# Kernel tuning notes

Measured on AMD Instinct MI355X. Metric: run time of the kernel, lower is better.

The kernel has to match this reference:

```python
import jax, jax.numpy as jnp
import numpy as np

H = 12
D_MODEL = 768
D_K = D_MODEL // H  # 64


def setup_inputs() -> dict:
    key = jax.random.key(0)
    ks = jax.random.split(key, 16)
    B, S, D = 4, 1024, D_MODEL
    scale = 1.0 / np.sqrt(D)
    inp = {
        "query": jax.random.normal(ks[0], (B, S, D), jnp.float32),
        "key": jax.random.normal(ks[1], (B, S, D), jnp.float32),
        "value": jax.random.normal(ks[2], (B, S, D), jnp.float32),
        "times": jax.random.normal(ks[3], (2, B, S, D), jnp.float32),
        # learned params (Linear weights stored torch-style [out, in])
        "Wq": jax.random.normal(ks[4], (D, D), jnp.float32) * scale,
        "bq": jnp.zeros((D,), jnp.float32),
        "Wk": jax.random.normal(ks[5], (D, D), jnp.float32) * scale,
        "bk": jnp.zeros((D,), jnp.float32),
        "Wv": jax.random.normal(ks[6], (D, D), jnp.float32) * scale,
        "bv": jnp.zeros((D,), jnp.float32),
        "Wt": jax.random.normal(ks[7], (D, D), jnp.float32) * scale,
        "bt": jnp.zeros((D,), jnp.float32),
        "Wo": jax.random.normal(ks[8], (D, D), jnp.float32) * scale,
        "bo": jnp.zeros((D,), jnp.float32),
    }
    return inp


def _split_heads(x, B, S):
    # [B,S,D] -> [B,H,S,D_K]
    return x.reshape(B, S, H, D_K).transpose(0, 2, 1, 3)


def reference(query, key, value, times, Wq, bq, Wk, bk, Wv, bv, Wt, bt, Wo, bo):
    B, S, D = query.shape
    inv_sqrt_dk = 1.0 / jnp.sqrt(jnp.asarray(D_K, query.dtype))
    # q/k/v projections are identical across time-loop iterations; hoist them.
    q = _split_heads(query @ Wq.T + bq, B, S)   # [B,H,S,dk]
    k = _split_heads(key @ Wk.T + bk, B, S)
    v = _split_heads(value @ Wv.T + bv, B, S)
    x = jnp.zeros_like(q)
    n_times = times.shape[0]
    for i in range(n_times):  # small fixed loop over time embeddings
        t = _split_heads(times[i] @ Wt.T + bt, B, S)
        # dual-score attention: query.time + query.key, each scaled by 1/sqrt(d_k)
        scores = (jnp.einsum('bhqd,bhkd->bhqk', q, t)
                  + jnp.einsum('bhqd,bhkd->bhqk', q, k)) * inv_sqrt_dk
        p = jax.nn.softmax(scores, axis=-1)
        x = x + jnp.einsum('bhqk,bhkd->bhqd', p, v)
    x = x.transpose(0, 2, 1, 3).reshape(B, S, H * D_K)
    return x @ Wo.T + bo
```

## Files before the change

kernel.cpp:

```cpp
#include <hip/hip_runtime.h>
#include <hip/hip_fp16.h>

typedef _Float16 v8h __attribute__((ext_vector_type(8)));
typedef _Float16 v4h __attribute__((ext_vector_type(4)));
typedef _Float16 v2h __attribute__((ext_vector_type(2)));
typedef float v4f __attribute__((ext_vector_type(4)));

#define MFMA_F16 __builtin_amdgcn_mfma_f32_16x16x32_f16
#define EXP2F __builtin_amdgcn_exp2f

__device__ static inline v2h pkrtz(float a, float b) {
  return __builtin_bit_cast(v2h, __builtin_amdgcn_cvt_pkrtz(a, b));
}

__device__ static inline void async_copy16(const void* g, void* l) {
  __builtin_amdgcn_global_load_lds(
      (const __attribute__((address_space(1))) void*)g,
      (__attribute__((address_space(3))) void*)l, 16, 0, 0);
}

struct CastArgs {
  const float* src[10];
  _Float16* dst[10];
  int start[11];
  float scale[10];
};
__global__ void cast_all(CastArgs a) {
  const int g = blockIdx.x * 256 + threadIdx.x;
  if (g >= a.start[10]) return;
  int z = 0;
  #pragma unroll
  for (int i = 1; i < 10; ++i) if (g >= a.start[i]) z = i;
  const int i0 = g - a.start[z];
  const float sc = a.scale[z];
  const float* s = a.src[z] + (size_t)i0 * 8;
  const float4 f0 = *(const float4*)s;
  const float4 f1 = *(const float4*)(s + 4);
  v8h o = {(_Float16)(f0.x * sc), (_Float16)(f0.y * sc),
           (_Float16)(f0.z * sc), (_Float16)(f0.w * sc),
           (_Float16)(f1.x * sc), (_Float16)(f1.y * sc),
           (_Float16)(f1.z * sc), (_Float16)(f1.w * sc)};
  *(v8h*)(a.dst[z] + (size_t)i0 * 8) = o;
}

struct GemmArgs {
  const _Float16* A1[4]; const _Float16* A2[4];
  const _Float16* W1[4]; const _Float16* W2[4];
  const float* b1[4];    const float* b2[4];
  void* out[4];
  float bscale[4];
  int K[4];
  int mode[4];
};

template <int MT>
__global__ __launch_bounds__(256) void gemm_mt(GemmArgs g) {
  constexpr int iA = MT / 32;
  constexpr int NMT = MT / 32;
  __shared__ _Float16 a_lds[MT * 64];
  __shared__ _Float16 w_lds[128 * 64];
  const int z = blockIdx.z;
  const int KK = g.K[z];
  const int tid = threadIdx.x;
  const int w = tid >> 6, lane = tid & 63, quad = lane >> 4, l16 = lane & 15;
  const int m0 = blockIdx.x * MT, n0 = blockIdx.y * 128;
  const int wm = (w >> 1) * (MT / 2), wn = (w & 1) * 64;

  size_t srcOff[4]; int ldsOff[4];
  #pragma unroll
  for (int i = 0; i < 4; ++i) {
    const int c = i * 256 + tid, row = c >> 3, slot = c & 7;
    srcOff[i] = (size_t)row * 768 + (size_t)((slot ^ (row & 7)) * 8);
    ldsOff[i] = (i * 256 + w * 64) * 8;
  }

  v4f acc[NMT][4] = {};

  for (int k0 = 0; k0 < KK; k0 += 64) {
    const _Float16* Asrc = (k0 < 768) ? g.A1[z] : g.A2[z];
    const _Float16* Wsrc = (k0 < 768) ? g.W1[z] : g.W2[z];
    const int kc = (k0 < 768) ? k0 : k0 - 768;
    __syncthreads();
    #pragma unroll
    for (int i = 0; i < 4; ++i) {
      if (i < iA)
        async_copy16(Asrc + (size_t)m0 * 768 + kc + srcOff[i], &a_lds[ldsOff[i]]);
      async_copy16(Wsrc + (size_t)n0 * 768 + kc + srcOff[i], &w_lds[ldsOff[i]]);
    }
    __syncthreads();

    #pragma unroll
    for (int kh = 0; kh < 2; ++kh) {
      v8h af[NMT], bf[4];
      #pragma unroll
      for (int mt = 0; mt < NMT; ++mt) {
        const int r = wm + mt * 16 + l16;
        af[mt] = *(const v8h*)&a_lds[r * 64 + (((kh * 4 + quad) ^ (r & 7)) * 8)];
      }
      #pragma unroll
      for (int nt = 0; nt < 4; ++nt) {
        const int r = wn + nt * 16 + l16;
        bf[nt] = *(const v8h*)&w_lds[r * 64 + (((kh * 4 + quad) ^ (r & 7)) * 8)];
      }
      #pragma unroll
      for (int mt = 0; mt < NMT; ++mt)
        #pragma unroll
        for (int nt = 0; nt < 4; ++nt)
          acc[mt][nt] = MFMA_F16(af[mt], bf[nt], acc[mt][nt], 0, 0, 0);
    }
  }

  const int mode = g.mode[z];
  #pragma unroll
  for (int nt = 0; nt < 4; ++nt) {
    const int col = n0 + wn + nt * 16 + l16;
    float bv = g.b1[z][col] * g.bscale[z];
    if (g.b2[z]) bv += g.b2[z][col];
    if (mode == 1) {
      _Float16* outp = (_Float16*)g.out[z];
      const int h = col >> 6, dk = col & 63;
      #pragma unroll
      for (int mt = 0; mt < NMT; ++mt) {
        const int row = m0 + wm + mt * 16 + quad * 4;
        const int b = row >> 10, s = row & 1023;
        const int sp = (s & ~31) | ((s & 12) << 1) | ((s & 16) >> 2);
        v4h pack = {(_Float16)(acc[mt][nt][0] + bv), (_Float16)(acc[mt][nt][1] + bv),
                    (_Float16)(acc[mt][nt][2] + bv), (_Float16)(acc[mt][nt][3] + bv)};
        *(v4h*)&outp[(size_t)((b * 12 + h) * 64 + dk) * 1024 + sp] = pack;
      }
    } else {
      #pragma unroll
      for (int mt = 0; mt < NMT; ++mt)
        #pragma unroll
        for (int r = 0; r < 4; ++r) {
          const int row = m0 + wm + mt * 16 + quad * 4 + r;
          const float v = acc[mt][nt][r] + bv;
          if (mode == 2) ((float*)g.out[z])[(size_t)row * 768 + col] = v;
          else ((_Float16*)g.out[z])[(size_t)row * 768 + col] = (_Float16)v;
        }
    }
  }
}

__global__ __launch_bounds__(256) void attn(
    const _Float16* __restrict__ Q,
    const _Float16* __restrict__ KT0, const _Float16* __restrict__ KT1,
    const _Float16* __restrict__ Vt,
    _Float16* __restrict__ X)
{
  __shared__ _Float16 lds[6 * 4096];

  const int tid = threadIdx.x;
  const int w = tid >> 6, lane = tid & 63, quad = lane >> 4, l16 = lane & 15;

  const int orig = blockIdx.y * 16 + blockIdx.x;
  const int wgid = (orig & 7) * 96 + (orig >> 3);
  const int bh = wgid >> 4, q0 = (wgid & 15) * 64;
  const int b = bh / 12, h = bh % 12;
  const size_t base = (size_t)b * 1024 * 768 + h * 64;

  const _Float16* k0s = KT0 + base;
  const _Float16* k1s = KT1 + base;
  const _Float16* vs  = Vt + (size_t)bh * 64 * 1024;

  size_t ktOff[2], vOff[2]; int ldsOff[2];
  #pragma unroll
  for (int i = 0; i < 2; ++i) {
    const int c = i * 256 + w * 64 + lane, row = c >> 3, slot = c & 7;
    const int logical = slot ^ (row & 7);
    ktOff[i] = (size_t)row * 768 + (size_t)(logical * 8);
    vOff[i] = (size_t)row * 1024 + (size_t)(logical * 8);
    ldsOff[i] = c * 8;
  }
  auto stage = [&](int buf) {
    #pragma unroll
    for (int i = 0; i < 2; ++i) {
      async_copy16(k0s + ktOff[i], &lds[buf * 4096 + ldsOff[i]]);
      async_copy16(k1s + ktOff[i], &lds[8192 + buf * 4096 + ldsOff[i]]);
      async_copy16(vs + vOff[i], &lds[16384 + buf * 4096 + ldsOff[i]]);
    }
    k0s += 64 * 768; k1s += 64 * 768; vs += 64;
  };

  const _Float16* Qw = Q + base + (size_t)(q0 + w * 16) * 768;
  const v8h qf0 = *(const v8h*)(Qw + (size_t)l16 * 768 + quad * 8);
  const v8h qf1 = *(const v8h*)(Qw + (size_t)l16 * 768 + 32 + quad * 8);

  int ra0[4], ra1[4];
  #pragma unroll
  for (int t = 0; t < 4; ++t) {
    const int r = t * 16 + l16, rw = r & 7;
    ra0[t] = (r * 64 + ((quad ^ rw) * 8)) * 2;
    ra1[t] = ra0[t] ^ 64;
  }

  const _Float16 one = (_Float16)1.f;
  const v8h ones8 = {one, one, one, one, one, one, one, one};
  v4f o[2][4] = {};
  v4f osum[2] = {};

  auto body = [&](int B, bool doStage) {
    __syncthreads();
    if (doStage) stage((B == 0) ? 1 : 0);

    const char* L = (const char*)lds;

    v4f s[2][4];
    __builtin_amdgcn_s_setprio(1);
    #pragma unroll
    for (int kvt = 0; kvt < 4; ++kvt) {
      const v8h k00 = *(const v8h*)(L + B + ra0[kvt]);
      const v8h k01 = *(const v8h*)(L + B + ra1[kvt]);
      const v8h k10 = *(const v8h*)(L + 16384 + B + ra0[kvt]);
      const v8h k11 = *(const v8h*)(L + 16384 + B + ra1[kvt]);
      s[0][kvt] = MFMA_F16(k00, qf0, v4f{}, 0, 0, 0);
      s[0][kvt] = MFMA_F16(k01, qf1, s[0][kvt], 0, 0, 0);
      s[1][kvt] = MFMA_F16(k10, qf0, v4f{}, 0, 0, 0);
      s[1][kvt] = MFMA_F16(k11, qf1, s[1][kvt], 0, 0, 0);
    }
    __builtin_amdgcn_s_setprio(0);

    v8h pb8[2][2];
    #pragma unroll
    for (int t = 0; t < 2; ++t)
      #pragma unroll
      for (int gg = 0; gg < 2; ++gg) {
        const v4f sa = s[t][gg * 2], sb = s[t][gg * 2 + 1];
        const v2h a0 = pkrtz(EXP2F(sa[0]), EXP2F(sa[1]));
        const v2h a1 = pkrtz(EXP2F(sa[2]), EXP2F(sa[3]));
        const v2h b0 = pkrtz(EXP2F(sb[0]), EXP2F(sb[1]));
        const v2h b1 = pkrtz(EXP2F(sb[2]), EXP2F(sb[3]));
        pb8[t][gg] = v8h{a0[0], a0[1], a1[0], a1[1], b0[0], b0[1], b1[0], b1[1]};
        osum[t] = MFMA_F16(ones8, pb8[t][gg], osum[t], 0, 0, 0);
      }

    __builtin_amdgcn_s_setprio(1);
    #pragma unroll
    for (int dkt = 0; dkt < 4; ++dkt) {
      const v8h v0 = *(const v8h*)(L + 32768 + B + ra0[dkt]);
      const v8h v1 = *(const v8h*)(L + 32768 + B + ra1[dkt]);
      o[0][dkt] = MFMA_F16(v0, pb8[0][0], o[0][dkt], 0, 0, 0);
      o[0][dkt] = MFMA_F16(v1, pb8[0][1], o[0][dkt], 0, 0, 0);
      o[1][dkt] = MFMA_F16(v0, pb8[1][0], o[1][dkt], 0, 0, 0);
      o[1][dkt] = MFMA_F16(v1, pb8[1][1], o[1][dkt], 0, 0, 0);
    }
    __builtin_amdgcn_s_setprio(0);
  };

  stage(0);
  for (int it = 0; it < 7; ++it) {
    body(0, true);
    body(8192, true);
  }
  body(0, true);
  body(8192, false);

  const float i0 = 1.0f / osum[0][0], i1 = 1.0f / osum[1][0];

  _Float16* Xw = X + base + (size_t)(q0 + w * 16 + l16) * 768;
  #pragma unroll
  for (int dkt = 0; dkt < 4; ++dkt) {
    v4h pack;
    #pragma unroll
    for (int r = 0; r < 4; ++r)
      pack[r] = (_Float16)(o[0][dkt][r] * i0 + o[1][dkt][r] * i1);
    *(v4h*)&Xw[dkt * 16 + quad * 4] = pack;
  }
}

extern "C" void kernel_launch(void* const* d_in, const int* in_sizes, int n_in,
                              void* d_out, int out_size, void* d_ws, size_t ws_size,
                              hipStream_t stream) {
  const float* query = (const float*)d_in[0];
  const float* key   = (const float*)d_in[1];
  const float* value = (const float*)d_in[2];
  const float* times = (const float*)d_in[3];
  const float* Wq = (const float*)d_in[4];  const float* bq = (const float*)d_in[5];
  const float* Wk = (const float*)d_in[6];  const float* bk = (const float*)d_in[7];
  const float* Wv = (const float*)d_in[8];  const float* bv = (const float*)d_in[9];
  const float* Wt = (const float*)d_in[10]; const float* bt = (const float*)d_in[11];
  const float* Wo = (const float*)d_in[12]; const float* bo = (const float*)d_in[13];
  float* out = (float*)d_out;

  const size_t NELEM = (size_t)4096 * 768;
  const size_t WELEM = (size_t)768 * 768;
  const float QSCALE = 0.125f * 1.4426950408889634f;

  char* ws = (char*)d_ws;
  size_t off = 0;
  auto alloc = [&](size_t bytes) {
    void* p = ws + off; off += (bytes + 255) & ~(size_t)255; return p;
  };
  _Float16* qh  = (_Float16*)alloc(NELEM * 2);
  _Float16* kh  = (_Float16*)alloc(NELEM * 2);
  _Float16* vh  = (_Float16*)alloc(NELEM * 2);
  _Float16* wqh = (_Float16*)alloc(WELEM * 2);
  _Float16* wkh = (_Float16*)alloc(WELEM * 2);
  _Float16* wvh = (_Float16*)alloc(WELEM * 2);
  _Float16* wth = (_Float16*)alloc(WELEM * 2);
  _Float16* woh = (_Float16*)alloc(WELEM * 2);
  _Float16* Qh  = (_Float16*)alloc(NELEM * 2);
  _Float16* KT0 = (_Float16*)alloc(NELEM * 2);
  _Float16* KT1 = (_Float16*)alloc(NELEM * 2);
  _Float16* Vt  = (_Float16*)alloc(NELEM * 2);
  _Float16* t0h = (_Float16*)d_out;
  _Float16* t1h = t0h + NELEM;
  _Float16* Xh = qh;

  CastArgs ca = {};
  const int nA8 = (int)(NELEM / 8), nW8 = (int)(WELEM / 8);
  const float* csrc[10] = {query, key, value, times, times + NELEM, Wq, Wk, Wv, Wt, Wo};
  _Float16* cdst[10] = {qh, kh, vh, t0h, t1h, wqh, wkh, wvh, wth, woh};
  int acc8 = 0;
  for (int i = 0; i < 10; ++i) {
    ca.src[i] = csrc[i]; ca.dst[i] = cdst[i];
    ca.start[i] = acc8;
    acc8 += (i < 5) ? nA8 : nW8;
    ca.scale[i] = (i == 5) ? QSCALE : 1.0f;
  }
  ca.start[10] = acc8;
  cast_all<<<dim3((acc8 + 255) / 256), 256, 0, stream>>>(ca);

  GemmArgs pa = {};
  pa.A1[0] = t0h; pa.A2[0] = kh; pa.W1[0] = wth; pa.W2[0] = wkh;
  pa.b1[0] = bt; pa.b2[0] = bk; pa.out[0] = KT0; pa.bscale[0] = 1.0f;
  pa.K[0] = 1536; pa.mode[0] = 0;
  pa.A1[1] = t1h; pa.A2[1] = kh; pa.W1[1] = wth; pa.W2[1] = wkh;
  pa.b1[1] = bt; pa.b2[1] = bk; pa.out[1] = KT1; pa.bscale[1] = 1.0f;
  pa.K[1] = 1536; pa.mode[1] = 0;
  pa.A1[2] = qh; pa.A2[2] = qh; pa.W1[2] = wqh; pa.W2[2] = wqh;
  pa.b1[2] = bq; pa.b2[2] = nullptr; pa.out[2] = Qh; pa.bscale[2] = QSCALE;
  pa.K[2] = 768; pa.mode[2] = 0;
  pa.A1[3] = vh; pa.A2[3] = vh; pa.W1[3] = wvh; pa.W2[3] = wvh;
  pa.b1[3] = bv; pa.b2[3] = nullptr; pa.out[3] = Vt; pa.bscale[3] = 1.0f;
  pa.K[3] = 768; pa.mode[3] = 1;
  gemm_mt<128><<<dim3(32, 6, 4), 256, 0, stream>>>(pa);

  attn<<<dim3(16, 48), 256, 0, stream>>>(Qh, KT0, KT1, Vt, Xh);

  GemmArgs oa = {};
  oa.A1[0] = Xh; oa.A2[0] = Xh; oa.W1[0] = woh; oa.W2[0] = woh;
  oa.b1[0] = bo; oa.b2[0] = nullptr; oa.out[0] = out; oa.bscale[0] = 1.0f;
  oa.K[0] = 768; oa.mode[0] = 2;
  gemm_mt<64><<<dim3(64, 6, 1), 256, 0, stream>>>(oa);
}
```

Before: 228.6 us.

## Fuse fp32-to-fp16 activation cast into projection GEMM with double-buffered staging

Activations are no longer cast to fp16 in a separate pass. The projection GEMM now reads fp32 query/key/value/times directly, converting them in registers before writing to LDS, so the cast kernel only handles the weights. Both GEMM variants also get double-buffered LDS for W (and for A in the fp16 path), with the next tile prefetched while the current one is computed. This removes a full fp16 write and re-read of about 5 activation tensors. In exchange the GEMM issues fp32 global loads (twice the bytes per A tile), uses more registers, and adds an extra barrier per k-step.

```diff
diff --git a/kernel.cpp b/kernel.cpp
--- a/kernel.cpp
+++ b/kernel.cpp
@@ -20,17 +20,17 @@
 }
 
 struct CastArgs {
-  const float* src[10];
-  _Float16* dst[10];
-  int start[11];
-  float scale[10];
+  const float* src[5];
+  _Float16* dst[5];
+  int start[6];
+  float scale[5];
 };
 __global__ void cast_all(CastArgs a) {
   const int g = blockIdx.x * 256 + threadIdx.x;
-  if (g >= a.start[10]) return;
+  if (g >= a.start[5]) return;
   int z = 0;
   #pragma unroll
-  for (int i = 1; i < 10; ++i) if (g >= a.start[i]) z = i;
+  for (int i = 1; i < 5; ++i) if (g >= a.start[i]) z = i;
   const int i0 = g - a.start[z];
   const float sc = a.scale[z];
   const float* s = a.src[z] + (size_t)i0 * 8;
@@ -44,7 +44,7 @@
 }
 
 struct GemmArgs {
-  const _Float16* A1[4]; const _Float16* A2[4];
+  const void* A1[4]; const void* A2[4];
   const _Float16* W1[4]; const _Float16* W2[4];
   const float* b1[4];    const float* b2[4];
   void* out[4];
@@ -53,12 +53,12 @@
   int mode[4];
 };
 
-template <int MT>
+template <int MT, bool AF32>
 __global__ __launch_bounds__(256) void gemm_mt(GemmArgs g) {
-  constexpr int iA = MT / 32;
   constexpr int NMT = MT / 32;
-  __shared__ _Float16 a_lds[MT * 64];
-  __shared__ _Float16 w_lds[128 * 64];
+  constexpr int ASLOT = MT / 32;
+  __shared__ _Float16 a_lds[(AF32 ? 1 : 2) * MT * 64];
+  __shared__ _Float16 w_lds[2 * 128 * 64];
   const int z = blockIdx.z;
   const int KK = g.K[z];
   const int tid = threadIdx.x;
@@ -66,28 +66,91 @@
   const int m0 = blockIdx.x * MT, n0 = blockIdx.y * 128;
   const int wm = (w >> 1) * (MT / 2), wn = (w & 1) * 64;
 
-  size_t srcOff[4]; int ldsOff[4];
+  size_t srcOffW[4]; int ldsOffW[4];
   #pragma unroll
   for (int i = 0; i < 4; ++i) {
     const int c = i * 256 + tid, row = c >> 3, slot = c & 7;
-    srcOff[i] = (size_t)row * 768 + (size_t)((slot ^ (row & 7)) * 8);
-    ldsOff[i] = (i * 256 + w * 64) * 8;
-  }
+    srcOffW[i] = (size_t)row * 768 + (size_t)((slot ^ (row & 7)) * 8);
+    ldsOffW[i] = (i * 256 + w * 64) * 8;
+  }
+
+  auto stageW = [&](const _Float16* Wsrc, int kc, int buf) {
+    #pragma unroll
+    for (int i = 0; i < 4; ++i)
+      async_copy16(Wsrc + (size_t)n0 * 768 + kc + srcOffW[i],
+                   &w_lds[buf * 8192 + ldsOffW[i]]);
+  };
+  auto stageA16 = [&](const _Float16* Asrc, int kc, int buf) {
+    #pragma unroll
+    for (int i = 0; i < MT / 32; ++i)
+      async_copy16(Asrc + (size_t)m0 * 768 + kc + srcOffW[i],
+                   &a_lds[buf * MT * 64 + ldsOffW[i]]);
+  };
+
+  int rowA[ASLOT], colA[ASLOT], dstA[ASLOT];
+  float4 areg[ASLOT][2];
+  if constexpr (AF32) {
+    #pragma unroll
+    for (int i = 0; i < ASLOT; ++i) {
+      const int s = i * 256 + tid, row = s >> 3, slot = s & 7;
+      rowA[i] = row;
+      colA[i] = (slot ^ (row & 7)) * 8;
+      dstA[i] = s * 8;
+    }
+  }
+  auto loadA = [&](const float* Af, int kc) {
+    #pragma unroll
+    for (int i = 0; i < ASLOT; ++i) {
+      const float* p = Af + (size_t)(m0 + rowA[i]) * 768 + kc + colA[i];
+      areg[i][0] = *(const float4*)p;
+      areg[i][1] = *(const float4*)(p + 4);
+    }
+  };
+  auto writeA = [&]() {
+    #pragma unroll
+    for (int i = 0; i < ASLOT; ++i) {
+      const float4 f0 = areg[i][0], f1 = areg[i][1];
+      v8h o = {(_Float16)f0.x, (_Float16)f0.y, (_Float16)f0.z, (_Float16)f0.w,
+               (_Float16)f1.x, (_Float16)f1.y, (_Float16)f1.z, (_Float16)f1.w};
+      *(v8h*)&a_lds[dstA[i]] = o;
+    }
+  };
+
+  const void* A1 = g.A1[z]; const void* A2 = g.A2[z];
+  const _Float16* W1 = g.W1[z]; const _Float16* W2 = g.W2[z];
 
   v4f acc[NMT][4] = {};
 
+  if constexpr (AF32) loadA((const float*)A1, 0);
+  else stageA16((const _Float16*)A1, 0, 0);
+  stageW(W1, 0, 0);
+
+  int cur = 0;
   for (int k0 = 0; k0 < KK; k0 += 64) {
-    const _Float16* Asrc = (k0 < 768) ? g.A1[z] : g.A2[z];
-    const _Float16* Wsrc = (k0 < 768) ? g.W1[z] : g.W2[z];
-    const int kc = (k0 < 768) ? k0 : k0 - 768;
+    const int k0n = k0 + 64;
+    const bool has_next = k0n < KK;
+    const int kcn = (k0n < 768) ? k0n : k0n - 768;
+    const bool nfirst = k0n < 768;
+
     __syncthreads();
-    #pragma unroll
-    for (int i = 0; i < 4; ++i) {
-      if (i < iA)
-        async_copy16(Asrc + (size_t)m0 * 768 + kc + srcOff[i], &a_lds[ldsOff[i]]);
-      async_copy16(Wsrc + (size_t)n0 * 768 + kc + srcOff[i], &w_lds[ldsOff[i]]);
-    }
-    __syncthreads();
+
+    if constexpr (AF32) {
+      writeA();
+      __syncthreads();
+      if (has_next) {
+        loadA((const float*)(nfirst ? A1 : A2), kcn);
+        stageW(nfirst ? W1 : W2, kcn, cur ^ 1);
+      }
+    } else {
+      if (has_next) {
+        stageA16((const _Float16*)(nfirst ? A1 : A2), kcn, cur ^ 1);
+        stageW(nfirst ? W1 : W2, kcn, cur ^ 1);
+      }
+    }
+
+    const _Float16* al;
+    if constexpr (AF32) al = a_lds; else al = &a_lds[cur * MT * 64];
+    const _Float16* wl = &w_lds[cur * 8192];
 
     #pragma unroll
     for (int kh = 0; kh < 2; ++kh) {
@@ -95,12 +158,12 @@
       #pragma unroll
       for (int mt = 0; mt < NMT; ++mt) {
         const int r = wm + mt * 16 + l16;
-        af[mt] = *(const v8h*)&a_lds[r * 64 + (((kh * 4 + quad) ^ (r & 7)) * 8)];
+        af[mt] = *(const v8h*)&al[r * 64 + (((kh * 4 + quad) ^ (r & 7)) * 8)];
       }
       #pragma unroll
       for (int nt = 0; nt < 4; ++nt) {
         const int r = wn + nt * 16 + l16;
-        bf[nt] = *(const v8h*)&w_lds[r * 64 + (((kh * 4 + quad) ^ (r & 7)) * 8)];
+        bf[nt] = *(const v8h*)&wl[r * 64 + (((kh * 4 + quad) ^ (r & 7)) * 8)];
       }
       #pragma unroll
       for (int mt = 0; mt < NMT; ++mt)
@@ -108,6 +171,7 @@
         for (int nt = 0; nt < 4; ++nt)
           acc[mt][nt] = MFMA_F16(af[mt], bf[nt], acc[mt][nt], 0, 0, 0);
     }
+    cur ^= 1;
   }
 
   const int mode = g.mode[z];
@@ -291,9 +355,6 @@
   auto alloc = [&](size_t bytes) {
     void* p = ws + off; off += (bytes + 255) & ~(size_t)255; return p;
   };
-  _Float16* qh  = (_Float16*)alloc(NELEM * 2);
-  _Float16* kh  = (_Float16*)alloc(NELEM * 2);
-  _Float16* vh  = (_Float16*)alloc(NELEM * 2);
   _Float16* wqh = (_Float16*)alloc(WELEM * 2);
   _Float16* wkh = (_Float16*)alloc(WELEM * 2);
   _Float16* wvh = (_Float16*)alloc(WELEM * 2);
@@ -303,38 +364,36 @@
   _Float16* KT0 = (_Float16*)alloc(NELEM * 2);
   _Float16* KT1 = (_Float16*)alloc(NELEM * 2);
   _Float16* Vt  = (_Float16*)alloc(NELEM * 2);
-  _Float16* t0h = (_Float16*)d_out;
-  _Float16* t1h = t0h + NELEM;
-  _Float16* Xh = qh;
+  _Float16* Xh  = (_Float16*)alloc(NELEM * 2);
 
   CastArgs ca = {};
-  const int nA8 = (int)(NELEM / 8), nW8 = (int)(WELEM / 8);
-  const float* csrc[10] = {query, key, value, times, times + NELEM, Wq, Wk, Wv, Wt, Wo};
-  _Float16* cdst[10] = {qh, kh, vh, t0h, t1h, wqh, wkh, wvh, wth, woh};
+  const int nW8 = (int)(WELEM / 8);
+  const float* csrc[5] = {Wq, Wk, Wv, Wt, Wo};
+  _Float16* cdst[5] = {wqh, wkh, wvh, wth, woh};
   int acc8 = 0;
-  for (int i = 0; i < 10; ++i) {
+  for (int i = 0; i < 5; ++i) {
     ca.src[i] = csrc[i]; ca.dst[i] = cdst[i];
     ca.start[i] = acc8;
-    acc8 += (i < 5) ? nA8 : nW8;
-    ca.scale[i] = (i == 5) ? QSCALE : 1.0f;
-  }
-  ca.start[10] = acc8;
+    acc8 += nW8;
+    ca.scale[i] = (i == 0) ? QSCALE : 1.0f;
+  }
+  ca.start[5] = acc8;
   cast_all<<<dim3((acc8 + 255) / 256), 256, 0, stream>>>(ca);
 
   GemmArgs pa = {};
-  pa.A1[0] = t0h; pa.A2[0] = kh; pa.W1[0] = wth; pa.W2[0] = wkh;
+  pa.A1[0] = times;         pa.A2[0] = key; pa.W1[0] = wth; pa.W2[0] = wkh;
   pa.b1[0] = bt; pa.b2[0] = bk; pa.out[0] = KT0; pa.bscale[0] = 1.0f;
   pa.K[0] = 1536; pa.mode[0] = 0;
-  pa.A1[1] = t1h; pa.A2[1] = kh; pa.W1[1] = wth; pa.W2[1] = wkh;
+  pa.A1[1] = times + NELEM; pa.A2[1] = key; pa.W1[1] = wth; pa.W2[1] = wkh;
   pa.b1[1] = bt; pa.b2[1] = bk; pa.out[1] = KT1; pa.bscale[1] = 1.0f;
   pa.K[1] = 1536; pa.mode[1] = 0;
-  pa.A1[2] = qh; pa.A2[2] = qh; pa.W1[2] = wqh; pa.W2[2] = wqh;
+  pa.A1[2] = query; pa.A2[2] = query; pa.W1[2] = wqh; pa.W2[2] = wqh;
   pa.b1[2] = bq; pa.b2[2] = nullptr; pa.out[2] = Qh; pa.bscale[2] = QSCALE;
   pa.K[2] = 768; pa.mode[2] = 0;
-  pa.A1[3] = vh; pa.A2[3] = vh; pa.W1[3] = wvh; pa.W2[3] = wvh;
+  pa.A1[3] = value; pa.A2[3] = value; pa.W1[3] = wvh; pa.W2[3] = wvh;
   pa.b1[3] = bv; pa.b2[3] = nullptr; pa.out[3] = Vt; pa.bscale[3] = 1.0f;
   pa.K[3] = 768; pa.mode[3] = 1;
-  gemm_mt<128><<<dim3(32, 6, 4), 256, 0, stream>>>(pa);
+  gemm_mt<128, true><<<dim3(32, 6, 4), 256, 0, stream>>>(pa);
 
   attn<<<dim3(16, 48), 256, 0, stream>>>(Qh, KT0, KT1, Vt, Xh);
 
@@ -342,5 +401,5 @@
   oa.A1[0] = Xh; oa.A2[0] = Xh; oa.W1[0] = woh; oa.W2[0] = woh;
   oa.b1[0] = bo; oa.b2[0] = nullptr; oa.out[0] = out; oa.bscale[0] = 1.0f;
   oa.K[0] = 768; oa.mode[0] = 2;
-  gemm_mt<64><<<dim3(64, 6, 1), 256, 0, stream>>>(oa);
-}
+  gemm_mt<64, false><<<dim3(64, 6, 1), 256, 0, stream>>>(oa);
+}
```

After: 218.6 us. 4.4% less time.
